# Performance work log

Measured on AMD Instinct MI355X. Metric: run time of the kernel, lower is better.

Reference implementation:

```python
import jax, jax.numpy as jnp
import numpy as np

N, E = 50000, 500000
F_IN, F_OUT, H = 128, 16, 8  # in_features, out_features, n_head


def setup_inputs() -> dict:
    key = jax.random.key(0)
    k1, k2, k3, k4, k5, k6 = jax.random.split(key, 6)
    x = jax.random.normal(k1, (N, F_IN), dtype=jnp.float32)
    # xavier_normal with gain 1.414 (as in the torch init)
    w_std = 1.414 * np.sqrt(2.0 / (F_IN + F_OUT * H))
    weight = jax.random.normal(k2, (F_IN, F_OUT * H), dtype=jnp.float32) * w_std
    b_std = 1.414 * np.sqrt(2.0 / (F_OUT + H))
    bias = jax.random.normal(k3, (1, F_OUT, H), dtype=jnp.float32) * b_std
    a_std = 1.414 * np.sqrt(2.0 / (F_OUT + H))
    a2 = jax.random.normal(k4, (F_OUT, H), dtype=jnp.float32) * a_std
    edge_index = jax.random.randint(k5, (2, E), 0, N, dtype=jnp.int64)
    adj_vals = jax.random.uniform(k6, (E,), dtype=jnp.float32)
    return {"x": x, "edge_index": edge_index, "adj_vals": adj_vals,
            "weight": weight, "bias": bias, "a2": a2}


def _spmm(rows, cols, vals, X, n):
    # sparse (n,n) @ dense (n,d): gather source rows, scale, scatter-add to dest rows
    return jax.ops.segment_sum(vals[:, None] * X[cols], rows, num_segments=n)


def reference(x, edge_index, adj_vals, weight, bias, a2):
    n = x.shape[0]
    rows, cols = edge_index[0], edge_index[1]
    # support0: (N, F_OUT, H) -- torch .view(N, out_features, n_head)
    support0 = (x @ weight).reshape(n, F_OUT, H)
    mask = jnp.ones((n, 1, H), dtype=x.dtype)
    support = jnp.concatenate([support0, mask], axis=1)  # (N, F_OUT+1, H)
    # per-node, per-head attention scalar (softplus-like via sqrt)
    attn2 = jnp.einsum('aij,ij->aj', support[:, :-1, :], a2)  # (N, H)
    attn2 = attn2 + jnp.sqrt(attn2 * attn2 + 1.0)
    # post_attn_order = 1 iteration
    attn_support = (support * attn2[:, None, :]).reshape(n, (F_OUT + 1) * H)
    # pre_attn_order = 1 SpMM propagation (no APPNP)
    attn_support = _spmm(rows, cols, adj_vals, attn_support, n)
    support = attn_support.reshape(n, F_OUT + 1, H)
    # self-normalize by the propagated mask column
    output = support[:, :-1, :] / (support[:, -1:, :] + 1e-9)
    output = output + bias  # (N, F_OUT, H)
    return output.reshape(n, F_OUT * H)
```

## Files before the change

### kernel.cpp

```cpp
#include <hip/hip_runtime.h>
#include <hip/hip_bf16.h>


#define F 128
#define NH 8
#define GN 16
#define XS 136
#define ZS2 128
#define HE 4
#define CAP 64

typedef __attribute__((ext_vector_type(8))) short bf16x8;
typedef __attribute__((ext_vector_type(4))) float f32x4;

static __device__ __forceinline__ unsigned short f2bf(float f) {
    __hip_bfloat16 h = __float2bfloat16(f);
    return *(unsigned short*)&h;
}
static __device__ __forceinline__ float bf_lo(unsigned int u) { return __uint_as_float(u << 16); }
static __device__ __forceinline__ float bf_hi(unsigned int u) { return __uint_as_float(u & 0xFFFF0000u); }

__global__ __launch_bounds__(256)
void k_prep_w(const float* __restrict__ w, unsigned short* __restrict__ wt,
              int* __restrict__ cnt, int ncnt)
{
    int idx = blockIdx.x * 256 + threadIdx.x;
    int col = idx >> 7;
    int k   = idx & 127;
    wt[col * 128 + k] = f2bf(w[k * F + col]);
    for (int i = idx; i < ncnt; i += 64 * 256) cnt[i] = 0;
}

__global__ __launch_bounds__(128)
void k_gemm_hist(const float* __restrict__ x, const unsigned short* __restrict__ wt,
                 const float* __restrict__ a2, unsigned short* __restrict__ zm,
                 unsigned short* __restrict__ zk, int n,
                 const int* __restrict__ rows, const int* __restrict__ cols,
                 const float* __restrict__ vals, int* __restrict__ cnt,
                 int2* __restrict__ ce, int E, int G1, int G2)
{
    __shared__ __align__(16) unsigned short xls[GN * XS];
    __shared__ float part[2 * GN * 8];
    __shared__ float sarr[GN * 8];

    const int bid = blockIdx.x;
    const int t   = threadIdx.x;

    int gemm_id;
    {
        const int quota4 = G2 * 4;
        if (bid < quota4) {
            int q = bid >> 2, r = bid & 3;
            if (r == 3) {
                int base = (q * 128 + t) * HE;
                if (base < E) {
                    if (base + HE <= E) {
                        int4   r4 = *(const int4*)(rows + base);
                        int4   c4 = *(const int4*)(cols + base);
                        float4 v4 = *(const float4*)(vals + base);
                        int k0 = atomicAdd(&cnt[r4.x], 1);
                        int k1 = atomicAdd(&cnt[r4.y], 1);
                        int k2 = atomicAdd(&cnt[r4.z], 1);
                        int k3 = atomicAdd(&cnt[r4.w], 1);
                        ce[(long)r4.x * CAP + k0] = make_int2(c4.x, __float_as_int(v4.x));
                        ce[(long)r4.y * CAP + k1] = make_int2(c4.y, __float_as_int(v4.y));
                        ce[(long)r4.z * CAP + k2] = make_int2(c4.z, __float_as_int(v4.z));
                        ce[(long)r4.w * CAP + k3] = make_int2(c4.w, __float_as_int(v4.w));
                    } else {
                        for (int e = base; e < E; ++e) {
                            int rr = rows[e];
                            int kk = atomicAdd(&cnt[rr], 1);
                            ce[(long)rr * CAP + kk] = make_int2(cols[e], __float_as_int(vals[e]));
                        }
                    }
                }
                return;
            }
            gemm_id = 3 * q + r;
        } else {
            gemm_id = bid - G2;
        }
    }
    if (gemm_id >= G1) return;

    const int l  = t & 63;
    const int w  = t >> 6;
    const int lm = l & 15;
    const int lq = l >> 4;
    const int n0 = gemm_id * GN;

    #pragma unroll
    for (int i = 0; i < 4; ++i) {
        int idx  = i * 128 + t;
        int node = idx >> 5;
        int k0   = (idx & 31) * 4;
        int gn   = n0 + node;
        float4 v = (gn < n) ? *(const float4*)(x + (long)gn * F + k0)
                            : make_float4(0.f, 0.f, 0.f, 0.f);
        ushort4 h;
        h.x = f2bf(v.x); h.y = f2bf(v.y); h.z = f2bf(v.z); h.w = f2bf(v.w);
        *(ushort4*)(&xls[node * XS + k0]) = h;
    }
    __syncthreads();

    const int wc = w * 64;
    f32x4 acc[4];
    #pragma unroll
    for (int cf = 0; cf < 4; ++cf) acc[cf] = (f32x4){0.f, 0.f, 0.f, 0.f};

    #pragma unroll
    for (int ks = 0; ks < 4; ++ks) {
        const int koff = ks * 32 + lq * 8;
        bf16x8 ah = *(const bf16x8*)(&xls[lm * XS + koff]);
        #pragma unroll
        for (int cf = 0; cf < 4; ++cf) {
            bf16x8 bh = *(const bf16x8*)(wt + (wc + cf * 16 + lm) * 128 + koff);
            acc[cf] = __builtin_amdgcn_mfma_f32_16x16x32_bf16(ah, bh, acc[cf], 0, 0, 0);
        }
    }

    float a2v[4];
    #pragma unroll
    for (int cf = 0; cf < 4; ++cf) a2v[cf] = a2[wc + cf * 16 + lm];
    const int j = l & 7;

    #pragma unroll
    for (int r = 0; r < 4; ++r) {
        float pl = 0.f;
        #pragma unroll
        for (int cf = 0; cf < 4; ++cf) pl = fmaf(acc[cf][r], a2v[cf], pl);
        pl += __shfl_xor(pl, 8, 64);
        if ((l & 8) == 0) {
            int node = lq * 4 + r;
            part[(w * GN + node) * 8 + j] = pl;
        }
    }
    __syncthreads();

    {
        int node = t >> 3;
        int jj   = t & 7;
        float ts = part[(0 * GN + node) * 8 + jj] + part[(1 * GN + node) * 8 + jj];
        float s = ts + sqrtf(ts * ts + 1.0f);
        sarr[node * 8 + jj] = s;
        int gn = n0 + node;
        if (gn < n) zk[(long)gn * NH + jj] = f2bf(s);
    }
    __syncthreads();

    #pragma unroll
    for (int r = 0; r < 4; ++r) {
        int node = lq * 4 + r;
        float sv = sarr[node * 8 + j];
        #pragma unroll
        for (int cf = 0; cf < 4; ++cf) {
            int c = wc + cf * 16 + lm;
            xls[node * ZS2 + c] = f2bf(acc[cf][r] * sv);
        }
    }
    __syncthreads();

    {
        int rows_here = n - n0; if (rows_here > GN) rows_here = GN;
        int nvec = rows_here * 16;
        const uint4* srcv = (const uint4*)xls;
        uint4* dstv = (uint4*)(zm + (size_t)n0 * F);
        #pragma unroll
        for (int i = 0; i < 2; ++i) {
            int idx = i * 128 + t;
            if (idx < nvec) dstv[idx] = srcv[idx];
        }
    }
}

__global__ __launch_bounds__(256)
void k_spmm_pull(const int* __restrict__ cnt, const int2* __restrict__ ce,
                 const unsigned short* __restrict__ zm, const unsigned short* __restrict__ zk,
                 const float* __restrict__ bias, float* __restrict__ out, int n)
{
    const int grp  = (blockIdx.x * blockDim.x + threadIdx.x) >> 4;
    const int lane = threadIdx.x & 63;
    const int c16  = lane & 15;
    if (grp >= n) return;

    const int mq  = c16 & 3;
    const int deg = cnt[grp];
    const int2* cebase = ce + (long)grp * CAP;

    float az[8];
    #pragma unroll
    for (int k = 0; k < 8; ++k) az[k] = 0.f;
    float am0 = 0.f, am1 = 0.f;

    for (int e = 0; e < deg; e += 4) {
        int e1 = (e + 1 < deg) ? e + 1 : deg - 1;
        int e2 = (e + 2 < deg) ? e + 2 : deg - 1;
        int e3 = (e + 3 < deg) ? e + 3 : deg - 1;
        int2 p0 = cebase[e];
        int2 p1 = cebase[e1];
        int2 p2 = cebase[e2];
        int2 p3 = cebase[e3];
        float v0 = __int_as_float(p0.y);
        float v1 = (e + 1 < deg) ? __int_as_float(p1.y) : 0.f;
        float v2 = (e + 2 < deg) ? __int_as_float(p2.y) : 0.f;
        float v3 = (e + 3 < deg) ? __int_as_float(p3.y) : 0.f;
        uint4 d0 = ((const uint4*)zm)[(long)p0.x * 16 + c16];
        uint4 d1 = ((const uint4*)zm)[(long)p1.x * 16 + c16];
        uint4 d2 = ((const uint4*)zm)[(long)p2.x * 16 + c16];
        uint4 d3 = ((const uint4*)zm)[(long)p3.x * 16 + c16];
        unsigned int m0 = *(const unsigned int*)(zk + (long)p0.x * NH + 2 * mq);
        unsigned int m1 = *(const unsigned int*)(zk + (long)p1.x * NH + 2 * mq);
        unsigned int m2 = *(const unsigned int*)(zk + (long)p2.x * NH + 2 * mq);
        unsigned int m3 = *(const unsigned int*)(zk + (long)p3.x * NH + 2 * mq);

        az[0] = fmaf(v0, bf_lo(d0.x), az[0]);  az[1] = fmaf(v0, bf_hi(d0.x), az[1]);
        az[2] = fmaf(v0, bf_lo(d0.y), az[2]);  az[3] = fmaf(v0, bf_hi(d0.y), az[3]);
        az[4] = fmaf(v0, bf_lo(d0.z), az[4]);  az[5] = fmaf(v0, bf_hi(d0.z), az[5]);
        az[6] = fmaf(v0, bf_lo(d0.w), az[6]);  az[7] = fmaf(v0, bf_hi(d0.w), az[7]);
        am0   = fmaf(v0, bf_lo(m0), am0);      am1   = fmaf(v0, bf_hi(m0), am1);

        az[0] = fmaf(v1, bf_lo(d1.x), az[0]);  az[1] = fmaf(v1, bf_hi(d1.x), az[1]);
        az[2] = fmaf(v1, bf_lo(d1.y), az[2]);  az[3] = fmaf(v1, bf_hi(d1.y), az[3]);
        az[4] = fmaf(v1, bf_lo(d1.z), az[4]);  az[5] = fmaf(v1, bf_hi(d1.z), az[5]);
        az[6] = fmaf(v1, bf_lo(d1.w), az[6]);  az[7] = fmaf(v1, bf_hi(d1.w), az[7]);
        am0   = fmaf(v1, bf_lo(m1), am0);      am1   = fmaf(v1, bf_hi(m1), am1);

        az[0] = fmaf(v2, bf_lo(d2.x), az[0]);  az[1] = fmaf(v2, bf_hi(d2.x), az[1]);
        az[2] = fmaf(v2, bf_lo(d2.y), az[2]);  az[3] = fmaf(v2, bf_hi(d2.y), az[3]);
        az[4] = fmaf(v2, bf_lo(d2.z), az[4]);  az[5] = fmaf(v2, bf_hi(d2.z), az[5]);
        az[6] = fmaf(v2, bf_lo(d2.w), az[6]);  az[7] = fmaf(v2, bf_hi(d2.w), az[7]);
        am0   = fmaf(v2, bf_lo(m2), am0);      am1   = fmaf(v2, bf_hi(m2), am1);

        az[0] = fmaf(v3, bf_lo(d3.x), az[0]);  az[1] = fmaf(v3, bf_hi(d3.x), az[1]);
        az[2] = fmaf(v3, bf_lo(d3.y), az[2]);  az[3] = fmaf(v3, bf_hi(d3.y), az[3]);
        az[4] = fmaf(v3, bf_lo(d3.z), az[4]);  az[5] = fmaf(v3, bf_hi(d3.z), az[5]);
        az[6] = fmaf(v3, bf_lo(d3.w), az[6]);  az[7] = fmaf(v3, bf_hi(d3.w), az[7]);
        am0   = fmaf(v3, bf_lo(m3), am0);      am1   = fmaf(v3, bf_hi(m3), am1);
    }

    const int gb = lane & 48;
    float den[8];
    den[0] = __shfl(am0, gb + 0, 64);  den[1] = __shfl(am1, gb + 0, 64);
    den[2] = __shfl(am0, gb + 1, 64);  den[3] = __shfl(am1, gb + 1, 64);
    den[4] = __shfl(am0, gb + 2, 64);  den[5] = __shfl(am1, gb + 2, 64);
    den[6] = __shfl(am0, gb + 3, 64);  den[7] = __shfl(am1, gb + 3, 64);

    const float* bp = bias + 8 * c16;
    float4 b0v = *(const float4*)(bp);
    float4 b1v = *(const float4*)(bp + 4);
    float4 o0, o1;
    o0.x = az[0] / (den[0] + 1e-9f) + b0v.x;
    o0.y = az[1] / (den[1] + 1e-9f) + b0v.y;
    o0.z = az[2] / (den[2] + 1e-9f) + b0v.z;
    o0.w = az[3] / (den[3] + 1e-9f) + b0v.w;
    o1.x = az[4] / (den[4] + 1e-9f) + b1v.x;
    o1.y = az[5] / (den[5] + 1e-9f) + b1v.y;
    o1.z = az[6] / (den[6] + 1e-9f) + b1v.z;
    o1.w = az[7] / (den[7] + 1e-9f) + b1v.w;
    float* op = out + (long)grp * F + 8 * c16;
    *(float4*)(op)     = o0;
    *(float4*)(op + 4) = o1;
}

extern "C" void kernel_launch(void* const* d_in, const int* in_sizes, int n_in,
                              void* d_out, int out_size, void* d_ws, size_t ws_size,
                              hipStream_t stream)
{
    const float* x    = (const float*)d_in[0];
    const int*   ei   = (const int*)d_in[1];
    const float* vals = (const float*)d_in[2];
    const float* w    = (const float*)d_in[3];
    const float* bias = (const float*)d_in[4];
    const float* a2   = (const float*)d_in[5];
    float* out = (float*)d_out;

    const int N = in_sizes[0] / F;
    const int E = in_sizes[2];
    const int* rows = ei;
    const int* cols = ei + E;

    const int G1 = (N + GN - 1) / GN;
    const int G2 = (E + 128 * HE - 1) / (128 * HE);

    char* p = (char*)d_ws;
    unsigned short* zm = (unsigned short*)p;  p += (size_t)N * F * sizeof(unsigned short);
    unsigned short* zk = (unsigned short*)p;  p += (((size_t)N * NH * sizeof(unsigned short) + 255) & ~255ull);
    unsigned short* wt = (unsigned short*)p;  p += 128 * 128 * sizeof(unsigned short);
    int*   cnt      = (int*)p;    p += (((size_t)N + 64) * sizeof(int) + 255 & ~255ull);
    int2*  ce       = (int2*)p;

    k_prep_w<<<dim3(64), dim3(256), 0, stream>>>(w, wt, cnt, N);

    k_gemm_hist<<<dim3(G1 + G2), dim3(128), 0, stream>>>(x, wt, a2, zm, zk, N,
                                                         rows, cols, vals, cnt, ce,
                                                         E, G1, G2);

    dim3 b5(256), g5(((size_t)N * 16 + 255) / 256);
    k_spmm_pull<<<g5, b5, 0, stream>>>(cnt, ce, zm, zk, bias, out, N);
}
```

Measured before the change: 71.01 us.

## Enlarge GEMM tiles to 64 nodes per block, stage weights in LDS per warp

Each GEMM block now processes 64 nodes with 256 threads. Each wave owns 16 nodes and all 128 columns, so the attention reduction stays inside the wave and the cross-wave shared-memory passes and two barriers are removed. The bf16 weight matrix is pre-permuted into an MFMA-friendly layout and copied into LDS once per block instead of being read from global memory per fragment. Histogram blocks are interleaved 1:1 with GEMM blocks at 256 threads. Per-block LDS grows to roughly 49KB, which may reduce occupancy, and the weight copy is repeated in every block.

```diff
diff --git a/kernel.cpp b/kernel.cpp
--- a/kernel.cpp
+++ b/kernel.cpp
@@ -4,9 +4,8 @@
 
 #define F 128
 #define NH 8
-#define GN 16
+#define GN 64
 #define XS 136
-#define ZS2 128
 #define HE 4
 #define CAP 64
 
@@ -27,11 +26,14 @@
     int idx = blockIdx.x * 256 + threadIdx.x;
     int col = idx >> 7;
     int k   = idx & 127;
-    wt[col * 128 + k] = f2bf(w[k * F + col]);
+    int ks  = k >> 5;
+    int lq  = (k >> 3) & 3;
+    int e   = k & 7;
+    wt[(((ks * 4 + lq) * 128) + col) * 8 + e] = f2bf(w[k * F + col]);
     for (int i = idx; i < ncnt; i += 64 * 256) cnt[i] = 0;
 }
 
-__global__ __launch_bounds__(128)
+__global__ __launch_bounds__(256)
 void k_gemm_hist(const float* __restrict__ x, const unsigned short* __restrict__ wt,
                  const float* __restrict__ a2, unsigned short* __restrict__ zm,
                  unsigned short* __restrict__ zk, int n,
@@ -40,46 +42,42 @@
                  int2* __restrict__ ce, int E, int G1, int G2)
 {
     __shared__ __align__(16) unsigned short xls[GN * XS];
-    __shared__ float part[2 * GN * 8];
-    __shared__ float sarr[GN * 8];
+    __shared__ __align__(16) unsigned short wt_lds[16384];
 
     const int bid = blockIdx.x;
     const int t   = threadIdx.x;
 
     int gemm_id;
-    {
-        const int quota4 = G2 * 4;
-        if (bid < quota4) {
-            int q = bid >> 2, r = bid & 3;
-            if (r == 3) {
-                int base = (q * 128 + t) * HE;
-                if (base < E) {
-                    if (base + HE <= E) {
-                        int4   r4 = *(const int4*)(rows + base);
-                        int4   c4 = *(const int4*)(cols + base);
-                        float4 v4 = *(const float4*)(vals + base);
-                        int k0 = atomicAdd(&cnt[r4.x], 1);
-                        int k1 = atomicAdd(&cnt[r4.y], 1);
-                        int k2 = atomicAdd(&cnt[r4.z], 1);
-                        int k3 = atomicAdd(&cnt[r4.w], 1);
-                        ce[(long)r4.x * CAP + k0] = make_int2(c4.x, __float_as_int(v4.x));
-                        ce[(long)r4.y * CAP + k1] = make_int2(c4.y, __float_as_int(v4.y));
-                        ce[(long)r4.z * CAP + k2] = make_int2(c4.z, __float_as_int(v4.z));
-                        ce[(long)r4.w * CAP + k3] = make_int2(c4.w, __float_as_int(v4.w));
-                    } else {
-                        for (int e = base; e < E; ++e) {
-                            int rr = rows[e];
-                            int kk = atomicAdd(&cnt[rr], 1);
-                            ce[(long)rr * CAP + kk] = make_int2(cols[e], __float_as_int(vals[e]));
-                        }
+    if (bid < 2 * G2) {
+        if (bid & 1) {
+            int q = bid >> 1;
+            int base = (q * 256 + t) * HE;
+            if (base < E) {
+                if (base + HE <= E) {
+                    int4   r4 = *(const int4*)(rows + base);
+                    int4   c4 = *(const int4*)(cols + base);
+                    float4 v4 = *(const float4*)(vals + base);
+                    int k0 = atomicAdd(&cnt[r4.x], 1);
+                    int k1 = atomicAdd(&cnt[r4.y], 1);
+                    int k2 = atomicAdd(&cnt[r4.z], 1);
+                    int k3 = atomicAdd(&cnt[r4.w], 1);
+                    ce[(long)r4.x * CAP + k0] = make_int2(c4.x, __float_as_int(v4.x));
+                    ce[(long)r4.y * CAP + k1] = make_int2(c4.y, __float_as_int(v4.y));
+                    ce[(long)r4.z * CAP + k2] = make_int2(c4.z, __float_as_int(v4.z));
+                    ce[(long)r4.w * CAP + k3] = make_int2(c4.w, __float_as_int(v4.w));
+                } else {
+                    for (int e = base; e < E; ++e) {
+                        int rr = rows[e];
+                        int kk = atomicAdd(&cnt[rr], 1);
+                        ce[(long)rr * CAP + kk] = make_int2(cols[e], __float_as_int(vals[e]));
                     }
                 }
-                return;
             }
-            gemm_id = 3 * q + r;
-        } else {
-            gemm_id = bid - G2;
-        }
+            return;
+        }
+        gemm_id = bid >> 1;
+    } else {
+        gemm_id = bid - G2;
     }
     if (gemm_id >= G1) return;
 
@@ -88,10 +86,17 @@
     const int lm = l & 15;
     const int lq = l >> 4;
     const int n0 = gemm_id * GN;
-
-    #pragma unroll
-    for (int i = 0; i < 4; ++i) {
-        int idx  = i * 128 + t;
+    const int nw = n0 + w * 16;
+
+    {
+        const uint4* ws = (const uint4*)wt;
+        uint4* wd = (uint4*)wt_lds;
+        #pragma unroll
+        for (int i = 0; i < 8; ++i) wd[i * 256 + t] = ws[i * 256 + t];
+    }
+    #pragma unroll
+    for (int i = 0; i < 8; ++i) {
+        int idx  = i * 256 + t;
         int node = idx >> 5;
         int k0   = (idx & 31) * 4;
         int gn   = n0 + node;
@@ -103,72 +108,63 @@
     }
     __syncthreads();
 
-    const int wc = w * 64;
-    f32x4 acc[4];
-    #pragma unroll
-    for (int cf = 0; cf < 4; ++cf) acc[cf] = (f32x4){0.f, 0.f, 0.f, 0.f};
+    f32x4 acc[8];
+    #pragma unroll
+    for (int cf = 0; cf < 8; ++cf) acc[cf] = (f32x4){0.f, 0.f, 0.f, 0.f};
 
     #pragma unroll
     for (int ks = 0; ks < 4; ++ks) {
         const int koff = ks * 32 + lq * 8;
-        bf16x8 ah = *(const bf16x8*)(&xls[lm * XS + koff]);
-        #pragma unroll
-        for (int cf = 0; cf < 4; ++cf) {
-            bf16x8 bh = *(const bf16x8*)(wt + (wc + cf * 16 + lm) * 128 + koff);
+        bf16x8 ah = *(const bf16x8*)(&xls[(w * 16 + lm) * XS + koff]);
+        const unsigned short* wb = wt_lds + (size_t)((ks * 4 + lq) * 128) * 8;
+        #pragma unroll
+        for (int cf = 0; cf < 8; ++cf) {
+            bf16x8 bh = *(const bf16x8*)(wb + (cf * 16 + lm) * 8);
             acc[cf] = __builtin_amdgcn_mfma_f32_16x16x32_bf16(ah, bh, acc[cf], 0, 0, 0);
         }
     }
 
-    float a2v[4];
-    #pragma unroll
-    for (int cf = 0; cf < 4; ++cf) a2v[cf] = a2[wc + cf * 16 + lm];
-    const int j = l & 7;
-
+    float a2v[8];
+    #pragma unroll
+    for (int cf = 0; cf < 8; ++cf) a2v[cf] = a2[cf * 16 + lm];
+
+    float s4[4];
     #pragma unroll
     for (int r = 0; r < 4; ++r) {
         float pl = 0.f;
         #pragma unroll
-        for (int cf = 0; cf < 4; ++cf) pl = fmaf(acc[cf][r], a2v[cf], pl);
+        for (int cf = 0; cf < 8; ++cf) pl = fmaf(acc[cf][r], a2v[cf], pl);
         pl += __shfl_xor(pl, 8, 64);
-        if ((l & 8) == 0) {
-            int node = lq * 4 + r;
-            part[(w * GN + node) * 8 + j] = pl;
-        }
-    }
-    __syncthreads();
-
-    {
-        int node = t >> 3;
-        int jj   = t & 7;
-        float ts = part[(0 * GN + node) * 8 + jj] + part[(1 * GN + node) * 8 + jj];
-        float s = ts + sqrtf(ts * ts + 1.0f);
-        sarr[node * 8 + jj] = s;
-        int gn = n0 + node;
-        if (gn < n) zk[(long)gn * NH + jj] = f2bf(s);
-    }
-    __syncthreads();
+        s4[r] = pl + sqrtf(pl * pl + 1.0f);
+    }
+
+    if (lm < NH) {
+        #pragma unroll
+        for (int r = 0; r < 4; ++r) {
+            int gn = nw + lq * 4 + r;
+            if (gn < n) zk[(long)gn * NH + lm] = f2bf(s4[r]);
+        }
+    }
 
     #pragma unroll
     for (int r = 0; r < 4; ++r) {
         int node = lq * 4 + r;
-        float sv = sarr[node * 8 + j];
-        #pragma unroll
-        for (int cf = 0; cf < 4; ++cf) {
-            int c = wc + cf * 16 + lm;
-            xls[node * ZS2 + c] = f2bf(acc[cf][r] * sv);
-        }
-    }
-    __syncthreads();
+        #pragma unroll
+        for (int cf = 0; cf < 8; ++cf)
+            xls[(w * 16 + node) * XS + cf * 16 + lm] = f2bf(acc[cf][r] * s4[r]);
+    }
 
     {
-        int rows_here = n - n0; if (rows_here > GN) rows_here = GN;
-        int nvec = rows_here * 16;
-        const uint4* srcv = (const uint4*)xls;
-        uint4* dstv = (uint4*)(zm + (size_t)n0 * F);
-        #pragma unroll
-        for (int i = 0; i < 2; ++i) {
-            int idx = i * 128 + t;
-            if (idx < nvec) dstv[idx] = srcv[idx];
+        int rowsw = n - nw; if (rowsw > 16) rowsw = 16;
+        #pragma unroll
+        for (int i = 0; i < 4; ++i) {
+            int idx = i * 64 + l;
+            int row = idx >> 4;
+            int q   = idx & 15;
+            if (row < rowsw) {
+                uint4 v = *(const uint4*)(&xls[(w * 16 + row) * XS + q * 8]);
+                ((uint4*)(zm + (size_t)(nw + row) * F))[q] = v;
+            }
         }
     }
 }
@@ -280,18 +276,18 @@
     const int* cols = ei + E;
 
     const int G1 = (N + GN - 1) / GN;
-    const int G2 = (E + 128 * HE - 1) / (128 * HE);
+    const int G2 = (E + 256 * HE - 1) / (256 * HE);
 
     char* p = (char*)d_ws;
     unsigned short* zm = (unsigned short*)p;  p += (size_t)N * F * sizeof(unsigned short);
     unsigned short* zk = (unsigned short*)p;  p += (((size_t)N * NH * sizeof(unsigned short) + 255) & ~255ull);
     unsigned short* wt = (unsigned short*)p;  p += 128 * 128 * sizeof(unsigned short);
-    int*   cnt      = (int*)p;    p += (((size_t)N + 64) * sizeof(int) + 255 & ~255ull);
+    int*   cnt      = (int*)p;    p += (((size_t)N + 64) * sizeof(int) + 255) & ~255ull;
     int2*  ce       = (int2*)p;
 
     k_prep_w<<<dim3(64), dim3(256), 0, stream>>>(w, wt, cnt, N);
 
-    k_gemm_hist<<<dim3(G1 + G2), dim3(128), 0, stream>>>(x, wt, a2, zm, zk, N,
+    k_gemm_hist<<<dim3(G1 + G2), dim3(256), 0, stream>>>(x, wt, a2, zm, zk, N,
                                                          rows, cols, vals, cnt, ce,
                                                          E, G1, G2);
 
```

Result: faster. 66.49 us (-6.4%).
